# Performance work log

Hardware: AMD Instinct MI355X
Metric: run time of the kernel (lower is better)

The kernel has to match this reference:

```python
import jax, jax.numpy as jnp
import numpy as np

N = 50000      # node_each_graph
K = 16         # fixed neighbor degree
D_IN = 128     # in_feats
D_H = 128      # n_hidden
C = 8          # n_classes
N_GATED = 3    # n_layers - 1
EPS = 1e-5     # LayerNorm eps
CLAMP = 1e-5   # entropy clamp


def _layernorm(x):
    # LayerNorm over the full node vector, elementwise_affine=False
    m = jnp.mean(x)
    v = jnp.mean((x - m) ** 2)
    return (x - m) / jnp.sqrt(v + EPS)


def setup_inputs() -> dict:
    key = jax.random.key(0)
    ks = jax.random.split(key, 8)
    feat = jax.random.normal(ks[0], (N, D_IN), jnp.float32)
    neighbors = jax.random.randint(ks[1], (N, K), 0, N)  # int neighbor ids
    s = 1.0 / np.sqrt(D_H)
    W_gcn = jax.random.uniform(ks[2], (D_IN, D_H), jnp.float32, -s, s)
    b_gcn = jax.random.uniform(ks[3], (D_H,), jnp.float32, -s, s)
    Wy = jax.random.normal(ks[4], (D_H, C), jnp.float32) * 0.05
    by = jnp.zeros((C,), jnp.float32)
    tau1 = jnp.zeros((1,), jnp.float32)  # global_tau_1 (shared_tau=True)
    tau2 = jnp.zeros((1,), jnp.float32)  # global_tau_2
    Wc = jax.random.normal(ks[5], (D_H * N, C), jnp.float32) * 1e-3
    bc = jnp.zeros((C,), jnp.float32)
    return {"feat": feat, "W_gcn": W_gcn, "b_gcn": b_gcn, "Wy": Wy,
            "by": by, "tau1": tau1, "tau2": tau2, "Wc": Wc, "bc": bc,
            "neighbors": neighbors}


def reference(feat, W_gcn, b_gcn, Wy, by, tau1, tau2, Wc, bc, neighbors):
    # Layer 0: GCNLayer (no activation, no dropout)
    h = feat @ W_gcn                      # [N, D_H]
    h = h[neighbors].sum(axis=1) + b_gcn  # neighbor-sum aggregation

    old_z = jnp.float32(1.0)
    for _ in range(N_GATED):
        # logits = softmax(weight_y(h))
        logits = jax.nn.softmax(h @ Wy + by, axis=1)          # [N, C]
        # adaptive_reduce_func (n_degree hard-coded to 1 in source)
        nb_logits = logits[neighbors]                          # [N, K, C]
        pred = jnp.argmax(nb_logits, axis=2)                   # [N, K]
        center = jnp.argmax(logits, axis=1)                    # [N]
        f1 = jnp.sum(pred == center[:, None], axis=1).astype(jnp.float32)
        # class histogram per node (== torch.unique loop when all classes occur)
        cnts = jax.nn.one_hot(pred, C, dtype=jnp.float32).sum(axis=1)  # [N, C]
        cnts = jnp.clip(cnts, CLAMP, None)
        f2 = -jnp.sum(cnts * jnp.log(cnts), axis=1)
        f1 = jax.lax.stop_gradient(f1)
        f2 = jax.lax.stop_gradient(f2)
        norm_f1 = _layernorm(f1)
        norm_f2 = _layernorm(f2)
        z = jax.nn.sigmoid(-(norm_f1 - tau1[0])) * jax.nn.sigmoid(-(norm_f2 - tau2[0]))
        gate = jnp.minimum(old_z, z)                           # [N]
        agg = h[neighbors].sum(axis=1)                         # [N, D_H]
        h = h + gate[:, None] * agg                            # activation=None
        old_z = z

    out = h.reshape(1, -1) @ Wc + bc                           # [1, C]
    return out
```

## Files before the change

### kernel.cpp

```cpp
#include <hip/hip_runtime.h>
#include <math.h>

#define NN 50000
#define DD 128
#define KK 16
#define CC 8

#define A_OFF    0u
#define B_OFF    (NN*DD*4u)
#define CENT_OFF (2u*NN*DD*4u)
#define ZOLD_OFF (CENT_OFF + NN*4u)
#define F1_OFF   (ZOLD_OFF + NN*4u)
#define F2_OFF   (F1_OFF + NN*4u)
#define SU_OFF   (F2_OFF + NN*4u)
#define SD_OFF   (SU_OFF + 8u)
#define OACC_OFF (SD_OFF + 16u)

__global__ __launch_bounds__(256) void k_gemm(const float* __restrict__ feat,
    const float* __restrict__ W, float* __restrict__ A, double* __restrict__ oacc)
{
    __shared__ __align__(16) float sW[DD*DD];
    __shared__ float sF[64][DD+1];
    const int t = threadIdx.x;
    const int base = blockIdx.x * 64;
    if (blockIdx.x == 0 && t < CC) oacc[t] = 0.0;

    const float4* W4 = (const float4*)W;
    float4* sW4 = (float4*)sW;
    #pragma unroll
    for (int i = 0; i < 16; ++i) sW4[t + i*256] = W4[t + i*256];

    const float4* F4 = (const float4*)feat;
    #pragma unroll
    for (int e = t; e < 64*32; e += 256) {
        int row = e >> 5, q = e & 31;
        float4 v = make_float4(0.f,0.f,0.f,0.f);
        if (base + row < NN) v = F4[(size_t)(base + row)*32 + q];
        sF[row][q*4+0] = v.x; sF[row][q*4+1] = v.y;
        sF[row][q*4+2] = v.z; sF[row][q*4+3] = v.w;
    }
    __syncthreads();

    const int cg = t & 15;
    const int ng = t >> 4;
    const int cb = cg * 8;
    float acc[4][8];
    #pragma unroll
    for (int j=0;j<4;++j)
        #pragma unroll
        for (int c=0;c<8;++c) acc[j][c]=0.f;

    #pragma unroll 4
    for (int d = 0; d < DD; ++d) {
        float4 wa = *(const float4*)&sW[d*DD + cb];
        float4 wb = *(const float4*)&sW[d*DD + cb + 4];
        #pragma unroll
        for (int j=0;j<4;++j) {
            float f = sF[ng*4+j][d];
            acc[j][0] += f*wa.x; acc[j][1] += f*wa.y;
            acc[j][2] += f*wa.z; acc[j][3] += f*wa.w;
            acc[j][4] += f*wb.x; acc[j][5] += f*wb.y;
            acc[j][6] += f*wb.z; acc[j][7] += f*wb.w;
        }
    }
    #pragma unroll
    for (int j=0;j<4;++j) {
        int node = base + ng*4 + j;
        if (node < NN) {
            float4* dst = (float4*)&A[(size_t)node*DD + cb];
            dst[0] = make_float4(acc[j][0],acc[j][1],acc[j][2],acc[j][3]);
            dst[1] = make_float4(acc[j][4],acc[j][5],acc[j][6],acc[j][7]);
        }
    }
}

__global__ __launch_bounds__(256) void k_agg0(const float4* __restrict__ A4,
    const int* __restrict__ nb, const float* __restrict__ bg,
    float4* __restrict__ H4, float* __restrict__ zold)
{
    const int t = threadIdx.x;
    const int node = blockIdx.x*8 + (t>>5);
    const int q = t & 31;
    if (node >= NN) return;
    const int* nbi = nb + node*KK;
    int idx[KK];
    #pragma unroll
    for (int k=0;k<KK;++k) idx[k] = nbi[k];
    float4 acc = ((const float4*)bg)[q];
    #pragma unroll
    for (int k=0;k<KK;++k) {
        float4 v = A4[(size_t)idx[k]*32 + q];
        acc.x += v.x; acc.y += v.y; acc.z += v.z; acc.w += v.w;
    }
    H4[(size_t)node*32 + q] = acc;
    if (q == 0) zold[node] = 1.0f;
}

__global__ __launch_bounds__(256) void k_center(const float* __restrict__ H,
    const float* __restrict__ Wy, const float* __restrict__ by,
    int* __restrict__ center, unsigned* __restrict__ su, double* __restrict__ sd)
{
    const int t = threadIdx.x;
    if (blockIdx.x == 0) {
        if (t < 2) su[t] = 0u;
        if (t >= 2 && t < 4) sd[t-2] = 0.0;
    }
    __shared__ float sH[64][DD+1];
    __shared__ __align__(16) float sWy[DD*CC];
    __shared__ float sby[CC];
    const int base = blockIdx.x * 64;
    const float4* H4 = (const float4*)H;
    #pragma unroll
    for (int e = t; e < 64*32; e += 256) {
        int row = e >> 5, q = e & 31;
        float4 v = make_float4(0.f,0.f,0.f,0.f);
        if (base + row < NN) v = H4[(size_t)(base+row)*32 + q];
        sH[row][q*4+0] = v.x; sH[row][q*4+1] = v.y;
        sH[row][q*4+2] = v.z; sH[row][q*4+3] = v.w;
    }
    ((float4*)sWy)[t] = ((const float4*)Wy)[t & 255];
    if (t < CC) sby[t] = by[t];
    __syncthreads();

    const int nl = t >> 2;
    const int c0 = (t & 3) * 2;
    float a0 = 0.f, a1 = 0.f;
    #pragma unroll 8
    for (int d = 0; d < DD; ++d) {
        float f = sH[nl][d];
        a0 += f * sWy[d*CC + c0];
        a1 += f * sWy[d*CC + c0 + 1];
    }
    a0 += sby[c0]; a1 += sby[c0+1];
    float bv = a0; int bi = c0;
    if (a1 > bv) { bv = a1; bi = c0 + 1; }
    #pragma unroll
    for (int off = 1; off < 4; off <<= 1) {
        float ov = __shfl_xor(bv, off, 64);
        int   oi = __shfl_xor(bi, off, 64);
        if (ov > bv || (ov == bv && oi < bi)) { bv = ov; bi = oi; }
    }
    const int node = base + nl;
    if ((t & 3) == 0 && node < NN) center[node] = bi;
}

__global__ __launch_bounds__(256) void k_stats(const int* __restrict__ center,
    const int* __restrict__ nb, float* __restrict__ f1o, float* __restrict__ f2o,
    unsigned* __restrict__ su, double* __restrict__ sd)
{
    const int t = threadIdx.x;
    const int i = blockIdx.x*256 + t;
    unsigned uf1 = 0, uf1sq = 0;
    double df2 = 0.0, df2sq = 0.0;
    if (i < NN) {
        const int ci = center[i];
        const int* nbi = nb + i*KK;
        unsigned long long cnt = 0ull;
        #pragma unroll
        for (int k=0;k<KK;++k) {
            int p = center[nbi[k]];
            cnt += 1ull << (p*8);
        }
        unsigned c1 = (unsigned)((cnt >> (ci*8)) & 0xFFull);
        float f2 = 0.f;
        #pragma unroll
        for (int c=0;c<CC;++c) {
            float fc = (float)((cnt >> (c*8)) & 0xFFull);
            fc = fmaxf(fc, 1e-5f);
            f2 -= fc * logf(fc);
        }
        f1o[i] = (float)c1;
        f2o[i] = f2;
        uf1 = c1; uf1sq = c1*c1;
        df2 = (double)f2; df2sq = df2*df2;
    }
    #pragma unroll
    for (int off = 32; off > 0; off >>= 1) {
        uf1   += __shfl_down(uf1,   off, 64);
        uf1sq += __shfl_down(uf1sq, off, 64);
        df2   += __shfl_down(df2,   off, 64);
        df2sq += __shfl_down(df2sq, off, 64);
    }
    __shared__ unsigned r1[4], r1s[4];
    __shared__ double   r2[4], r2s[4];
    const int wid = t >> 6, lane = t & 63;
    if (lane == 0) { r1[wid]=uf1; r1s[wid]=uf1sq; r2[wid]=df2; r2s[wid]=df2sq; }
    __syncthreads();
    if (t == 0) {
        atomicAdd(&su[0], r1[0]+r1[1]+r1[2]+r1[3]);
        atomicAdd(&su[1], r1s[0]+r1s[1]+r1s[2]+r1s[3]);
        atomicAdd(&sd[0], r2[0]+r2[1]+r2[2]+r2[3]);
        atomicAdd(&sd[1], r2s[0]+r2s[1]+r2s[2]+r2s[3]);
    }
}

__global__ __launch_bounds__(256) void k_update(const float4* __restrict__ Hin4,
    float4* __restrict__ Hout4, const int* __restrict__ nb,
    const float* __restrict__ f1, const float* __restrict__ f2,
    float* __restrict__ zold, const unsigned* __restrict__ su,
    const double* __restrict__ sd, const float* __restrict__ tau1,
    const float* __restrict__ tau2)
{
    const int t = threadIdx.x;
    const int node = blockIdx.x*8 + (t>>5);
    const int q = t & 31;
    if (node >= NN) return;
    const double invN = 1.0 / (double)NN;
    double mu1  = (double)su[0] * invN;
    double var1 = (double)su[1] * invN - mu1*mu1;
    double is1  = 1.0 / sqrt(var1 + 1e-5);
    double mu2  = sd[0] * invN;
    double var2 = sd[1] * invN - mu2*mu2;
    double is2  = 1.0 / sqrt(var2 + 1e-5);
    float nf1 = (float)(((double)f1[node] - mu1) * is1);
    float nf2 = (float)(((double)f2[node] - mu2) * is2);
    float z = (1.0f/(1.0f + expf(nf1 - tau1[0]))) * (1.0f/(1.0f + expf(nf2 - tau2[0])));
    float gate = fminf(zold[node], z);
    if (q == 0) zold[node] = z;

    const int* nbi = nb + node*KK;
    int idx[KK];
    #pragma unroll
    for (int k=0;k<KK;++k) idx[k] = nbi[k];
    float4 acc = make_float4(0.f,0.f,0.f,0.f);
    #pragma unroll
    for (int k=0;k<KK;++k) {
        float4 v = Hin4[(size_t)idx[k]*32 + q];
        acc.x += v.x; acc.y += v.y; acc.z += v.z; acc.w += v.w;
    }
    float4 h = Hin4[(size_t)node*32 + q];
    h.x += gate*acc.x; h.y += gate*acc.y; h.z += gate*acc.z; h.w += gate*acc.w;
    Hout4[(size_t)node*32 + q] = h;
}

__global__ __launch_bounds__(256) void k_final(const float* __restrict__ H,
    const float4* __restrict__ Wc4, double* __restrict__ oacc)
{
    const int t = threadIdx.x;
    float a[8];
    #pragma unroll
    for (int c=0;c<8;++c) a[c]=0.f;
    const int R = NN*DD;
    for (int r = blockIdx.x*256 + t; r < R; r += gridDim.x*256) {
        float h = H[r];
        float4 wa = Wc4[(size_t)r*2], wb = Wc4[(size_t)r*2 + 1];
        a[0]+=h*wa.x; a[1]+=h*wa.y; a[2]+=h*wa.z; a[3]+=h*wa.w;
        a[4]+=h*wb.x; a[5]+=h*wb.y; a[6]+=h*wb.z; a[7]+=h*wb.w;
    }
    #pragma unroll
    for (int off = 32; off > 0; off >>= 1)
        #pragma unroll
        for (int c=0;c<8;++c) a[c] += __shfl_down(a[c], off, 64);
    __shared__ double sred[4][8];
    const int wid = t >> 6, lane = t & 63;
    if (lane == 0) {
        #pragma unroll
        for (int c=0;c<8;++c) sred[wid][c] = (double)a[c];
    }
    __syncthreads();
    if (t < 8) {
        double s = sred[0][t]+sred[1][t]+sred[2][t]+sred[3][t];
        atomicAdd(&oacc[t], s);
    }
}

__global__ void k_fin(const double* __restrict__ oacc, const float* __restrict__ bc,
                      float* __restrict__ out)
{
    const int t = threadIdx.x;
    if (t < CC) out[t] = (float)(oacc[t] + (double)bc[t]);
}

extern "C" void kernel_launch(void* const* d_in, const int* in_sizes, int n_in,
                              void* d_out, int out_size, void* d_ws, size_t ws_size,
                              hipStream_t stream)
{
    const float* feat = (const float*)d_in[0];
    const float* Wg   = (const float*)d_in[1];
    const float* bg   = (const float*)d_in[2];
    const float* Wy   = (const float*)d_in[3];
    const float* by   = (const float*)d_in[4];
    const float* tau1 = (const float*)d_in[5];
    const float* tau2 = (const float*)d_in[6];
    const float* Wc   = (const float*)d_in[7];
    const float* bc   = (const float*)d_in[8];
    const int*   nb   = (const int*)d_in[9];

    char* ws = (char*)d_ws;
    float*    A      = (float*)(ws + A_OFF);
    float*    B      = (float*)(ws + B_OFF);
    int*      center = (int*)(ws + CENT_OFF);
    float*    zold   = (float*)(ws + ZOLD_OFF);
    float*    f1     = (float*)(ws + F1_OFF);
    float*    f2     = (float*)(ws + F2_OFF);
    unsigned* su     = (unsigned*)(ws + SU_OFF);
    double*   sd     = (double*)(ws + SD_OFF);
    double*   oacc   = (double*)(ws + OACC_OFF);

    k_gemm<<<(NN + 63)/64, 256, 0, stream>>>(feat, Wg, A, oacc);
    k_agg0<<<(NN + 7)/8, 256, 0, stream>>>((const float4*)A, nb, bg, (float4*)B, zold);

    float* hcur = B; float* hnext = A;
    for (int it = 0; it < 3; ++it) {
        k_center<<<(NN + 63)/64, 256, 0, stream>>>(hcur, Wy, by, center, su, sd);
        k_stats<<<(NN + 255)/256, 256, 0, stream>>>(center, nb, f1, f2, su, sd);
        k_update<<<(NN + 7)/8, 256, 0, stream>>>((const float4*)hcur, (float4*)hnext,
                                                 nb, f1, f2, zold, su, sd, tau1, tau2);
        float* tmp = hcur; hcur = hnext; hnext = tmp;
    }
    k_final<<<2048, 256, 0, stream>>>(hcur, (const float4*)Wc, oacc);
    k_fin<<<1, 64, 0, stream>>>(oacc, bc, (float*)d_out);
}
```

Measured before the change: 663.7 us.

## Store hidden states in column-chunked layout for cache-friendly neighbor gathers

After: 591.5 us. -10.9%, faster.

```diff
diff --git a/kernel.cpp b/kernel.cpp
--- a/kernel.cpp
+++ b/kernel.cpp
@@ -5,12 +5,15 @@
 #define DD 128
 #define KK 16
 #define CC 8
+#define NCH 4
+#define NB_AGG 1563
 
 #define A_OFF    0u
 #define B_OFF    (NN*DD*4u)
 #define CENT_OFF (2u*NN*DD*4u)
-#define ZOLD_OFF (CENT_OFF + NN*4u)
-#define F1_OFF   (ZOLD_OFF + NN*4u)
+#define Z0_OFF   (CENT_OFF + NN*4u)
+#define Z1_OFF   (Z0_OFF + NN*4u)
+#define F1_OFF   (Z1_OFF + NN*4u)
 #define F2_OFF   (F1_OFF + NN*4u)
 #define SU_OFF   (F2_OFF + NN*4u)
 #define SD_OFF   (SU_OFF + 8u)
@@ -63,11 +66,13 @@
             acc[j][6] += f*wb.z; acc[j][7] += f*wb.w;
         }
     }
+    const int ch = cb >> 5;
+    const int co = cb & 31;
     #pragma unroll
     for (int j=0;j<4;++j) {
         int node = base + ng*4 + j;
         if (node < NN) {
-            float4* dst = (float4*)&A[(size_t)node*DD + cb];
+            float4* dst = (float4*)&A[((size_t)ch*NN + node)*32 + co];
             dst[0] = make_float4(acc[j][0],acc[j][1],acc[j][2],acc[j][3]);
             dst[1] = make_float4(acc[j][4],acc[j][5],acc[j][6],acc[j][7]);
         }
@@ -79,21 +84,27 @@
     float4* __restrict__ H4, float* __restrict__ zold)
 {
     const int t = threadIdx.x;
-    const int node = blockIdx.x*8 + (t>>5);
-    const int q = t & 31;
+    const int c = blockIdx.x / NB_AGG;
+    const int nbase = (blockIdx.x % NB_AGG) * 32;
+    __shared__ int sIdx[32*KK];
+    if (t < 128) {
+        if (nbase + (t >> 2) < NN)
+            ((int4*)sIdx)[t] = ((const int4*)(nb + (size_t)nbase*KK))[t];
+    }
+    __syncthreads();
+    const int nl = t >> 3;
+    const int q  = t & 7;
+    const int node = nbase + nl;
     if (node >= NN) return;
-    const int* nbi = nb + node*KK;
-    int idx[KK];
-    #pragma unroll
-    for (int k=0;k<KK;++k) idx[k] = nbi[k];
-    float4 acc = ((const float4*)bg)[q];
+    float4 acc = ((const float4*)bg)[c*8 + q];
     #pragma unroll
     for (int k=0;k<KK;++k) {
-        float4 v = A4[(size_t)idx[k]*32 + q];
+        int idx = sIdx[nl*KK + k];
+        float4 v = A4[((size_t)c*NN + idx)*8 + q];
         acc.x += v.x; acc.y += v.y; acc.z += v.z; acc.w += v.w;
     }
-    H4[(size_t)node*32 + q] = acc;
-    if (q == 0) zold[node] = 1.0f;
+    H4[((size_t)c*NN + node)*8 + q] = acc;
+    if (c == 0 && q == 0) zold[node] = 1.0f;
 }
 
 __global__ __launch_bounds__(256) void k_center(const float* __restrict__ H,
@@ -113,8 +124,9 @@
     #pragma unroll
     for (int e = t; e < 64*32; e += 256) {
         int row = e >> 5, q = e & 31;
+        int ch = q >> 3, q8 = q & 7;
         float4 v = make_float4(0.f,0.f,0.f,0.f);
-        if (base + row < NN) v = H4[(size_t)(base+row)*32 + q];
+        if (base + row < NN) v = H4[((size_t)ch*NN + base+row)*8 + q8];
         sH[row][q*4+0] = v.x; sH[row][q*4+1] = v.y;
         sH[row][q*4+2] = v.z; sH[row][q*4+3] = v.w;
     }
@@ -197,14 +209,24 @@
 __global__ __launch_bounds__(256) void k_update(const float4* __restrict__ Hin4,
     float4* __restrict__ Hout4, const int* __restrict__ nb,
     const float* __restrict__ f1, const float* __restrict__ f2,
-    float* __restrict__ zold, const unsigned* __restrict__ su,
-    const double* __restrict__ sd, const float* __restrict__ tau1,
-    const float* __restrict__ tau2)
-{
-    const int t = threadIdx.x;
-    const int node = blockIdx.x*8 + (t>>5);
-    const int q = t & 31;
+    const float* __restrict__ zr, float* __restrict__ zw,
+    const unsigned* __restrict__ su, const double* __restrict__ sd,
+    const float* __restrict__ tau1, const float* __restrict__ tau2)
+{
+    const int t = threadIdx.x;
+    const int c = blockIdx.x / NB_AGG;
+    const int nbase = (blockIdx.x % NB_AGG) * 32;
+    __shared__ int sIdx[32*KK];
+    if (t < 128) {
+        if (nbase + (t >> 2) < NN)
+            ((int4*)sIdx)[t] = ((const int4*)(nb + (size_t)nbase*KK))[t];
+    }
+    __syncthreads();
+    const int nl = t >> 3;
+    const int q  = t & 7;
+    const int node = nbase + nl;
     if (node >= NN) return;
+
     const double invN = 1.0 / (double)NN;
     double mu1  = (double)su[0] * invN;
     double var1 = (double)su[1] * invN - mu1*mu1;
@@ -215,22 +237,19 @@
     float nf1 = (float)(((double)f1[node] - mu1) * is1);
     float nf2 = (float)(((double)f2[node] - mu2) * is2);
     float z = (1.0f/(1.0f + expf(nf1 - tau1[0]))) * (1.0f/(1.0f + expf(nf2 - tau2[0])));
-    float gate = fminf(zold[node], z);
-    if (q == 0) zold[node] = z;
-
-    const int* nbi = nb + node*KK;
-    int idx[KK];
-    #pragma unroll
-    for (int k=0;k<KK;++k) idx[k] = nbi[k];
+    float gate = fminf(zr[node], z);
+    if (c == 0 && q == 0) zw[node] = z;
+
     float4 acc = make_float4(0.f,0.f,0.f,0.f);
     #pragma unroll
     for (int k=0;k<KK;++k) {
-        float4 v = Hin4[(size_t)idx[k]*32 + q];
+        int idx = sIdx[nl*KK + k];
+        float4 v = Hin4[((size_t)c*NN + idx)*8 + q];
         acc.x += v.x; acc.y += v.y; acc.z += v.z; acc.w += v.w;
     }
-    float4 h = Hin4[(size_t)node*32 + q];
+    float4 h = Hin4[((size_t)c*NN + node)*8 + q];
     h.x += gate*acc.x; h.y += gate*acc.y; h.z += gate*acc.z; h.w += gate*acc.w;
-    Hout4[(size_t)node*32 + q] = h;
+    Hout4[((size_t)c*NN + node)*8 + q] = h;
 }
 
 __global__ __launch_bounds__(256) void k_final(const float* __restrict__ H,
@@ -242,7 +261,8 @@
     for (int c=0;c<8;++c) a[c]=0.f;
     const int R = NN*DD;
     for (int r = blockIdx.x*256 + t; r < R; r += gridDim.x*256) {
-        float h = H[r];
+        int node = r >> 7, d = r & 127;
+        float h = H[(((d>>5)*NN + node) << 5) + (d & 31)];
         float4 wa = Wc4[(size_t)r*2], wb = Wc4[(size_t)r*2 + 1];
         a[0]+=h*wa.x; a[1]+=h*wa.y; a[2]+=h*wa.z; a[3]+=h*wa.w;
         a[4]+=h*wb.x; a[5]+=h*wb.y; a[6]+=h*wb.z; a[7]+=h*wb.w;
@@ -290,7 +310,8 @@
     float*    A      = (float*)(ws + A_OFF);
     float*    B      = (float*)(ws + B_OFF);
     int*      center = (int*)(ws + CENT_OFF);
-    float*    zold   = (float*)(ws + ZOLD_OFF);
+    float*    z0     = (float*)(ws + Z0_OFF);
+    float*    z1     = (float*)(ws + Z1_OFF);
     float*    f1     = (float*)(ws + F1_OFF);
     float*    f2     = (float*)(ws + F2_OFF);
     unsigned* su     = (unsigned*)(ws + SU_OFF);
@@ -298,15 +319,17 @@
     double*   oacc   = (double*)(ws + OACC_OFF);
 
     k_gemm<<<(NN + 63)/64, 256, 0, stream>>>(feat, Wg, A, oacc);
-    k_agg0<<<(NN + 7)/8, 256, 0, stream>>>((const float4*)A, nb, bg, (float4*)B, zold);
+    k_agg0<<<NCH*NB_AGG, 256, 0, stream>>>((const float4*)A, nb, bg, (float4*)B, z0);
 
     float* hcur = B; float* hnext = A;
+    float* zcur = z0; float* znext = z1;
     for (int it = 0; it < 3; ++it) {
         k_center<<<(NN + 63)/64, 256, 0, stream>>>(hcur, Wy, by, center, su, sd);
         k_stats<<<(NN + 255)/256, 256, 0, stream>>>(center, nb, f1, f2, su, sd);
-        k_update<<<(NN + 7)/8, 256, 0, stream>>>((const float4*)hcur, (float4*)hnext,
-                                                 nb, f1, f2, zold, su, sd, tau1, tau2);
+        k_update<<<NCH*NB_AGG, 256, 0, stream>>>((const float4*)hcur, (float4*)hnext,
+                                                 nb, f1, f2, zcur, znext, su, sd, tau1, tau2);
         float* tmp = hcur; hcur = hnext; hnext = tmp;
+        tmp = zcur; zcur = znext; znext = tmp;
     }
     k_final<<<2048, 256, 0, stream>>>(hcur, (const float4*)Wc, oacc);
     k_fin<<<1, 64, 0, stream>>>(oacc, bc, (float*)d_out);
```

## Chunk hidden features by column blocks and fuse center argmax into aggregation

Applied to the files above, without the earlier changes.

New measurement: 620.4 us. 1.07x faster.

```diff
diff --git a/kernel.cpp b/kernel.cpp
--- a/kernel.cpp
+++ b/kernel.cpp
@@ -5,25 +5,32 @@
 #define DD 128
 #define KK 16
 #define CC 8
+#define NCH 8
+#define NB64 782
 
 #define A_OFF    0u
 #define B_OFF    (NN*DD*4u)
 #define CENT_OFF (2u*NN*DD*4u)
-#define ZOLD_OFF (CENT_OFF + NN*4u)
-#define F1_OFF   (ZOLD_OFF + NN*4u)
+#define Z0_OFF   (CENT_OFF + NN*4u)
+#define Z1_OFF   (Z0_OFF + NN*4u)
+#define F1_OFF   (Z1_OFF + NN*4u)
 #define F2_OFF   (F1_OFF + NN*4u)
 #define SU_OFF   (F2_OFF + NN*4u)
-#define SD_OFF   (SU_OFF + 8u)
-#define OACC_OFF (SD_OFF + 16u)
+#define SD_OFF   (SU_OFF + 32u)
+#define OACC_OFF (SD_OFF + 48u)
 
 __global__ __launch_bounds__(256) void k_gemm(const float* __restrict__ feat,
-    const float* __restrict__ W, float* __restrict__ A, double* __restrict__ oacc)
+    const float* __restrict__ W, float* __restrict__ A, double* __restrict__ oacc,
+    unsigned* __restrict__ su, double* __restrict__ sd)
 {
     __shared__ __align__(16) float sW[DD*DD];
     __shared__ float sF[64][DD+1];
     const int t = threadIdx.x;
     const int base = blockIdx.x * 64;
-    if (blockIdx.x == 0 && t < CC) oacc[t] = 0.0;
+    if (blockIdx.x == 0) {
+        if (t < 8) oacc[t] = 0.0;
+        if (t < 6) { su[t] = 0u; sd[t] = 0.0; }
+    }
 
     const float4* W4 = (const float4*)W;
     float4* sW4 = (float4*)sW;
@@ -63,11 +70,13 @@
             acc[j][6] += f*wb.z; acc[j][7] += f*wb.w;
         }
     }
+    const int ch = cb >> 4;
+    const int co = cb & 15;
     #pragma unroll
     for (int j=0;j<4;++j) {
         int node = base + ng*4 + j;
         if (node < NN) {
-            float4* dst = (float4*)&A[(size_t)node*DD + cb];
+            float4* dst = (float4*)&A[((size_t)ch*NN + node)*16 + co];
             dst[0] = make_float4(acc[j][0],acc[j][1],acc[j][2],acc[j][3]);
             dst[1] = make_float4(acc[j][4],acc[j][5],acc[j][6],acc[j][7]);
         }
@@ -76,77 +85,63 @@
 
 __global__ __launch_bounds__(256) void k_agg0(const float4* __restrict__ A4,
     const int* __restrict__ nb, const float* __restrict__ bg,
-    float4* __restrict__ H4, float* __restrict__ zold)
-{
-    const int t = threadIdx.x;
-    const int node = blockIdx.x*8 + (t>>5);
-    const int q = t & 31;
-    if (node >= NN) return;
-    const int* nbi = nb + node*KK;
-    int idx[KK];
-    #pragma unroll
-    for (int k=0;k<KK;++k) idx[k] = nbi[k];
-    float4 acc = ((const float4*)bg)[q];
-    #pragma unroll
-    for (int k=0;k<KK;++k) {
-        float4 v = A4[(size_t)idx[k]*32 + q];
-        acc.x += v.x; acc.y += v.y; acc.z += v.z; acc.w += v.w;
-    }
-    H4[(size_t)node*32 + q] = acc;
-    if (q == 0) zold[node] = 1.0f;
-}
-
-__global__ __launch_bounds__(256) void k_center(const float* __restrict__ H,
-    const float* __restrict__ Wy, const float* __restrict__ by,
-    int* __restrict__ center, unsigned* __restrict__ su, double* __restrict__ sd)
-{
-    const int t = threadIdx.x;
-    if (blockIdx.x == 0) {
-        if (t < 2) su[t] = 0u;
-        if (t >= 2 && t < 4) sd[t-2] = 0.0;
-    }
-    __shared__ float sH[64][DD+1];
+    const float4* __restrict__ Wy4, const float* __restrict__ by,
+    float4* __restrict__ H4, float* __restrict__ zold, int* __restrict__ center)
+{
     __shared__ __align__(16) float sWy[DD*CC];
     __shared__ float sby[CC];
-    const int base = blockIdx.x * 64;
-    const float4* H4 = (const float4*)H;
-    #pragma unroll
-    for (int e = t; e < 64*32; e += 256) {
-        int row = e >> 5, q = e & 31;
-        float4 v = make_float4(0.f,0.f,0.f,0.f);
-        if (base + row < NN) v = H4[(size_t)(base+row)*32 + q];
-        sH[row][q*4+0] = v.x; sH[row][q*4+1] = v.y;
-        sH[row][q*4+2] = v.z; sH[row][q*4+3] = v.w;
-    }
-    ((float4*)sWy)[t] = ((const float4*)Wy)[t & 255];
+    const int t = threadIdx.x;
+    ((float4*)sWy)[t] = Wy4[t];
     if (t < CC) sby[t] = by[t];
     __syncthreads();
-
-    const int nl = t >> 2;
-    const int c0 = (t & 3) * 2;
-    float a0 = 0.f, a1 = 0.f;
-    #pragma unroll 8
-    for (int d = 0; d < DD; ++d) {
-        float f = sH[nl][d];
-        a0 += f * sWy[d*CC + c0];
-        a1 += f * sWy[d*CC + c0 + 1];
-    }
-    a0 += sby[c0]; a1 += sby[c0+1];
-    float bv = a0; int bi = c0;
-    if (a1 > bv) { bv = a1; bi = c0 + 1; }
-    #pragma unroll
-    for (int off = 1; off < 4; off <<= 1) {
-        float ov = __shfl_xor(bv, off, 64);
-        int   oi = __shfl_xor(bi, off, 64);
-        if (ov > bv || (ov == bv && oi < bi)) { bv = ov; bi = oi; }
-    }
-    const int node = base + nl;
-    if ((t & 3) == 0 && node < NN) center[node] = bi;
+    const int nl = t >> 2, q = t & 3;
+    const int node = blockIdx.x*64 + nl;
+    if (node >= NN) return;
+
+    int idx[KK];
+    const int4* nbv = (const int4*)(nb + (size_t)node*KK);
+    #pragma unroll
+    for (int k4 = 0; k4 < 4; ++k4) {
+        int4 v = nbv[k4];
+        idx[k4*4+0]=v.x; idx[k4*4+1]=v.y; idx[k4*4+2]=v.z; idx[k4*4+3]=v.w;
+    }
+    float lg[CC];
+    #pragma unroll
+    for (int c=0;c<CC;++c) lg[c]=0.f;
+
+    for (int c = 0; c < NCH; ++c) {
+        float4 acc = ((const float4*)bg)[c*4 + q];
+        #pragma unroll
+        for (int k=0;k<KK;++k) {
+            float4 v = A4[((size_t)c*NN + idx[k])*4 + q];
+            acc.x += v.x; acc.y += v.y; acc.z += v.z; acc.w += v.w;
+        }
+        H4[((size_t)c*NN + node)*4 + q] = acc;
+        const int d0 = c*16 + q*4;
+        #pragma unroll
+        for (int cls=0; cls<CC; ++cls)
+            lg[cls] += acc.x*sWy[(d0+0)*CC+cls] + acc.y*sWy[(d0+1)*CC+cls]
+                     + acc.z*sWy[(d0+2)*CC+cls] + acc.w*sWy[(d0+3)*CC+cls];
+    }
+    #pragma unroll
+    for (int off=1; off<4; off<<=1)
+        #pragma unroll
+        for (int cls=0; cls<CC; ++cls) lg[cls] += __shfl_xor(lg[cls], off, 64);
+    if (q == 0) {
+        float bv = lg[0] + sby[0]; int bi = 0;
+        #pragma unroll
+        for (int cls=1; cls<CC; ++cls) {
+            float v = lg[cls] + sby[cls];
+            if (v > bv) { bv = v; bi = cls; }
+        }
+        center[node] = bi;
+        zold[node] = 1.0f;
+    }
 }
 
 __global__ __launch_bounds__(256) void k_stats(const int* __restrict__ center,
     const int* __restrict__ nb, float* __restrict__ f1o, float* __restrict__ f2o,
-    unsigned* __restrict__ su, double* __restrict__ sd)
+    unsigned* __restrict__ su2, double* __restrict__ sd2)
 {
     const int t = threadIdx.x;
     const int i = blockIdx.x*256 + t;
@@ -187,50 +182,85 @@
     if (lane == 0) { r1[wid]=uf1; r1s[wid]=uf1sq; r2[wid]=df2; r2s[wid]=df2sq; }
     __syncthreads();
     if (t == 0) {
-        atomicAdd(&su[0], r1[0]+r1[1]+r1[2]+r1[3]);
-        atomicAdd(&su[1], r1s[0]+r1s[1]+r1s[2]+r1s[3]);
-        atomicAdd(&sd[0], r2[0]+r2[1]+r2[2]+r2[3]);
-        atomicAdd(&sd[1], r2s[0]+r2s[1]+r2s[2]+r2s[3]);
+        atomicAdd(&su2[0], r1[0]+r1[1]+r1[2]+r1[3]);
+        atomicAdd(&su2[1], r1s[0]+r1s[1]+r1s[2]+r1s[3]);
+        atomicAdd(&sd2[0], r2[0]+r2[1]+r2[2]+r2[3]);
+        atomicAdd(&sd2[1], r2s[0]+r2s[1]+r2s[2]+r2s[3]);
     }
 }
 
 __global__ __launch_bounds__(256) void k_update(const float4* __restrict__ Hin4,
     float4* __restrict__ Hout4, const int* __restrict__ nb,
     const float* __restrict__ f1, const float* __restrict__ f2,
-    float* __restrict__ zold, const unsigned* __restrict__ su,
-    const double* __restrict__ sd, const float* __restrict__ tau1,
-    const float* __restrict__ tau2)
-{
-    const int t = threadIdx.x;
-    const int node = blockIdx.x*8 + (t>>5);
-    const int q = t & 31;
+    const float* __restrict__ zr, float* __restrict__ zw,
+    const unsigned* __restrict__ su2, const double* __restrict__ sd2,
+    const float* __restrict__ tau1, const float* __restrict__ tau2,
+    const float4* __restrict__ Wy4, const float* __restrict__ by,
+    int* __restrict__ center)
+{
+    __shared__ __align__(16) float sWy[DD*CC];
+    __shared__ float sby[CC];
+    const int t = threadIdx.x;
+    ((float4*)sWy)[t] = Wy4[t];
+    if (t < CC) sby[t] = by[t];
+    __syncthreads();
+    const int nl = t >> 2, q = t & 3;
+    const int node = blockIdx.x*64 + nl;
     if (node >= NN) return;
+
     const double invN = 1.0 / (double)NN;
-    double mu1  = (double)su[0] * invN;
-    double var1 = (double)su[1] * invN - mu1*mu1;
+    double mu1  = (double)su2[0] * invN;
+    double var1 = (double)su2[1] * invN - mu1*mu1;
     double is1  = 1.0 / sqrt(var1 + 1e-5);
-    double mu2  = sd[0] * invN;
-    double var2 = sd[1] * invN - mu2*mu2;
+    double mu2  = sd2[0] * invN;
+    double var2 = sd2[1] * invN - mu2*mu2;
     double is2  = 1.0 / sqrt(var2 + 1e-5);
     float nf1 = (float)(((double)f1[node] - mu1) * is1);
     float nf2 = (float)(((double)f2[node] - mu2) * is2);
     float z = (1.0f/(1.0f + expf(nf1 - tau1[0]))) * (1.0f/(1.0f + expf(nf2 - tau2[0])));
-    float gate = fminf(zold[node], z);
-    if (q == 0) zold[node] = z;
-
-    const int* nbi = nb + node*KK;
+    float gate = fminf(zr[node], z);
+    if (q == 0) zw[node] = z;
+
     int idx[KK];
-    #pragma unroll
-    for (int k=0;k<KK;++k) idx[k] = nbi[k];
-    float4 acc = make_float4(0.f,0.f,0.f,0.f);
-    #pragma unroll
-    for (int k=0;k<KK;++k) {
-        float4 v = Hin4[(size_t)idx[k]*32 + q];
-        acc.x += v.x; acc.y += v.y; acc.z += v.z; acc.w += v.w;
-    }
-    float4 h = Hin4[(size_t)node*32 + q];
-    h.x += gate*acc.x; h.y += gate*acc.y; h.z += gate*acc.z; h.w += gate*acc.w;
-    Hout4[(size_t)node*32 + q] = h;
+    const int4* nbv = (const int4*)(nb + (size_t)node*KK);
+    #pragma unroll
+    for (int k4 = 0; k4 < 4; ++k4) {
+        int4 v = nbv[k4];
+        idx[k4*4+0]=v.x; idx[k4*4+1]=v.y; idx[k4*4+2]=v.z; idx[k4*4+3]=v.w;
+    }
+    float lg[CC];
+    #pragma unroll
+    for (int c=0;c<CC;++c) lg[c]=0.f;
+
+    for (int c = 0; c < NCH; ++c) {
+        float4 acc = make_float4(0.f,0.f,0.f,0.f);
+        #pragma unroll
+        for (int k=0;k<KK;++k) {
+            float4 v = Hin4[((size_t)c*NN + idx[k])*4 + q];
+            acc.x += v.x; acc.y += v.y; acc.z += v.z; acc.w += v.w;
+        }
+        float4 h = Hin4[((size_t)c*NN + node)*4 + q];
+        h.x += gate*acc.x; h.y += gate*acc.y; h.z += gate*acc.z; h.w += gate*acc.w;
+        Hout4[((size_t)c*NN + node)*4 + q] = h;
+        const int d0 = c*16 + q*4;
+        #pragma unroll
+        for (int cls=0; cls<CC; ++cls)
+            lg[cls] += h.x*sWy[(d0+0)*CC+cls] + h.y*sWy[(d0+1)*CC+cls]
+                     + h.z*sWy[(d0+2)*CC+cls] + h.w*sWy[(d0+3)*CC+cls];
+    }
+    #pragma unroll
+    for (int off=1; off<4; off<<=1)
+        #pragma unroll
+        for (int cls=0; cls<CC; ++cls) lg[cls] += __shfl_xor(lg[cls], off, 64);
+    if (q == 0) {
+        float bv = lg[0] + sby[0]; int bi = 0;
+        #pragma unroll
+        for (int cls=1; cls<CC; ++cls) {
+            float v = lg[cls] + sby[cls];
+            if (v > bv) { bv = v; bi = cls; }
+        }
+        center[node] = bi;
+    }
 }
 
 __global__ __launch_bounds__(256) void k_final(const float* __restrict__ H,
@@ -240,12 +270,19 @@
     float a[8];
     #pragma unroll
     for (int c=0;c<8;++c) a[c]=0.f;
-    const int R = NN*DD;
-    for (int r = blockIdx.x*256 + t; r < R; r += gridDim.x*256) {
-        float h = H[r];
-        float4 wa = Wc4[(size_t)r*2], wb = Wc4[(size_t)r*2 + 1];
-        a[0]+=h*wa.x; a[1]+=h*wa.y; a[2]+=h*wa.z; a[3]+=h*wa.w;
-        a[4]+=h*wb.x; a[5]+=h*wb.y; a[6]+=h*wb.z; a[7]+=h*wb.w;
+    const int E = NN*DD/4;
+    for (int e = blockIdx.x*256 + t; e < E; e += gridDim.x*256) {
+        int r = e*4;
+        int node = r >> 7, d = r & 127;
+        float4 h4 = *(const float4*)&H[(((size_t)(d>>4)*NN + node) << 4) + (d & 15)];
+        float hh[4] = {h4.x, h4.y, h4.z, h4.w};
+        #pragma unroll
+        for (int j=0;j<4;++j) {
+            float h = hh[j];
+            float4 wa = Wc4[(size_t)(r+j)*2], wb = Wc4[(size_t)(r+j)*2 + 1];
+            a[0]+=h*wa.x; a[1]+=h*wa.y; a[2]+=h*wa.z; a[3]+=h*wa.w;
+            a[4]+=h*wb.x; a[5]+=h*wb.y; a[6]+=h*wb.z; a[7]+=h*wb.w;
+        }
     }
     #pragma unroll
     for (int off = 32; off > 0; off >>= 1)
@@ -290,23 +327,27 @@
     float*    A      = (float*)(ws + A_OFF);
     float*    B      = (float*)(ws + B_OFF);
     int*      center = (int*)(ws + CENT_OFF);
-    float*    zold   = (float*)(ws + ZOLD_OFF);
+    float*    z0     = (float*)(ws + Z0_OFF);
+    float*    z1     = (float*)(ws + Z1_OFF);
     float*    f1     = (float*)(ws + F1_OFF);
     float*    f2     = (float*)(ws + F2_OFF);
     unsigned* su     = (unsigned*)(ws + SU_OFF);
     double*   sd     = (double*)(ws + SD_OFF);
     double*   oacc   = (double*)(ws + OACC_OFF);
 
-    k_gemm<<<(NN + 63)/64, 256, 0, stream>>>(feat, Wg, A, oacc);
-    k_agg0<<<(NN + 7)/8, 256, 0, stream>>>((const float4*)A, nb, bg, (float4*)B, zold);
+    k_gemm<<<NB64, 256, 0, stream>>>(feat, Wg, A, oacc, su, sd);
+    k_agg0<<<NB64, 256, 0, stream>>>((const float4*)A, nb, bg, (const float4*)Wy, by,
+                                     (float4*)B, z0, center);
 
     float* hcur = B; float* hnext = A;
+    float* zcur = z0; float* znext = z1;
     for (int it = 0; it < 3; ++it) {
-        k_center<<<(NN + 63)/64, 256, 0, stream>>>(hcur, Wy, by, center, su, sd);
-        k_stats<<<(NN + 255)/256, 256, 0, stream>>>(center, nb, f1, f2, su, sd);
-        k_update<<<(NN + 7)/8, 256, 0, stream>>>((const float4*)hcur, (float4*)hnext,
-                                                 nb, f1, f2, zold, su, sd, tau1, tau2);
+        k_stats<<<(NN + 255)/256, 256, 0, stream>>>(center, nb, f1, f2, su + 2*it, sd + 2*it);
+        k_update<<<NB64, 256, 0, stream>>>((const float4*)hcur, (float4*)hnext, nb,
+                                           f1, f2, zcur, znext, su + 2*it, sd + 2*it,
+                                           tau1, tau2, (const float4*)Wy, by, center);
         float* tmp = hcur; hcur = hnext; hnext = tmp;
+        tmp = zcur; zcur = znext; znext = tmp;
     }
     k_final<<<2048, 256, 0, stream>>>(hcur, (const float4*)Wc, oacc);
     k_fin<<<1, 64, 0, stream>>>(oacc, bc, (float*)d_out);
```
